# Performance work log

Measured on AMD Instinct MI355X. Metric: run time of the kernel, lower is better.

The kernel has to match this reference:

```python
import jax, jax.numpy as jnp
import numpy as np

N = 50000   # nodes
E = 800000  # edges
F = 256     # input features
H = 256     # hidden units
L = 128     # n_labels
EPS = 1e-5


def setup_inputs():
    key = jax.random.key(0)
    ks = jax.random.split(key, 17)
    s = 0.05
    return {
        "features": jax.random.normal(ks[0], (N, F), jnp.float32),
        "edge_vals": jax.random.uniform(ks[1], (E,), jnp.float32),
        "W1": jax.random.normal(ks[2], (F, H), jnp.float32) * s,
        "db1": jax.random.normal(ks[3], (H,), jnp.float32) * s,
        "b1": jax.random.normal(ks[4], (H,), jnp.float32) * s,
        "g1": jax.random.uniform(ks[5], (H,), jnp.float32, 0.5, 1.5),
        "be1": jax.random.normal(ks[6], (H,), jnp.float32) * s,
        "W2": jax.random.normal(ks[7], (H, H), jnp.float32) * s,
        "b2": jax.random.normal(ks[8], (H,), jnp.float32) * s,
        "g2": jax.random.uniform(ks[9], (H,), jnp.float32, 0.5, 1.5),
        "be2": jax.random.normal(ks[10], (H,), jnp.float32) * s,
        "Wf": jax.random.normal(ks[11], (H, L), jnp.float32) * s,
        "bf": jax.random.normal(ks[12], (L,), jnp.float32) * s,
        "edge_rows": jax.random.randint(ks[13], (E,), 0, N, jnp.int32),
        "edge_cols": jax.random.randint(ks[14], (E,), 0, N, jnp.int32),
        "idx": jax.random.randint(ks[15], (N // 2,), 0, N, jnp.int32),
    }


def _spmm(edge_vals, rows, cols, x):
    # out[i] = sum_{(i,j) in E} A[i,j] * x[j]  (COO sparse @ dense)
    return jax.ops.segment_sum(edge_vals[:, None] * x[cols], rows, num_segments=N)


def _bn(x, gamma, beta):
    # training-mode BatchNormalization: batch (population) stats over nodes
    m = jnp.mean(x, axis=0)
    v = jnp.var(x, axis=0)
    return (x - m) * jax.lax.rsqrt(v + EPS) * gamma + beta


def reference(features, edge_vals, W1, db1, b1, g1, be1, W2, b2, g2, be2, Wf, bf,
              edge_rows, edge_cols, idx):
    # layer 1 (Dense has bias only for l == 0)
    h = features @ W1 + db1
    h = _spmm(edge_vals, edge_rows, edge_cols, h) + b1
    h = jax.nn.relu(_bn(h, g1, be1))
    # layer 2 (no dense bias)
    h = h @ W2
    h = _spmm(edge_vals, edge_rows, edge_cols, h) + b2
    h = jax.nn.relu(_bn(h, g2, be2))
    # dropout = identity (deterministic baseline); final dense head
    out = h @ Wf + bf
    return out[idx]
```

## Files before the change

kernel.cpp:

```cpp
#include <hip/hip_runtime.h>
#include <stdint.h>

#define NN 50000
#define EE 800000
#define FF 256
#define HH 256
#define LL 128
#define SBLK 1024
#define CSRCAP 1000448

typedef __bf16 bf16x8 __attribute__((ext_vector_type(8)));
typedef float  f32x4  __attribute__((ext_vector_type(4)));
typedef unsigned int u32x2 __attribute__((ext_vector_type(2)));
typedef unsigned int u32x4 __attribute__((ext_vector_type(4)));

typedef __attribute__((address_space(1))) unsigned int uint_as1;
typedef __attribute__((address_space(3))) unsigned int uint_as3;

__device__ __forceinline__ unsigned short f2bf(float f) {
  union { float f; unsigned int u; } v; v.f = f;
  unsigned int u = v.u;
  u += 0x7FFFu + ((u >> 16) & 1u);
  return (unsigned short)(u >> 16);
}

__device__ __forceinline__ float bf2f(unsigned short u) {
  union { unsigned int u; float f; } v;
  v.u = ((unsigned int)u) << 16;
  return v.f;
}

__device__ __forceinline__ f32x4 bf4_to_f32(ushort4 u) {
  f32x4 r;
  r.x = bf2f(u.x); r.y = bf2f(u.y); r.z = bf2f(u.z); r.w = bf2f(u.w);
  return r;
}

__device__ __forceinline__ void gload_lds16(const void* g, void* l) {
  __builtin_amdgcn_global_load_lds((const uint_as1*)g, (uint_as3*)l, 16, 0, 0);
}

__global__ __launch_bounds__(256) void k_setup(const int* __restrict__ erows,
                                               int* __restrict__ cnt,
                                               const float* __restrict__ features,
                                               unsigned short* __restrict__ Xb,
                                               const float* __restrict__ W1,
                                               unsigned short* __restrict__ W1t,
                                               const float* __restrict__ W2,
                                               unsigned short* __restrict__ W2t,
                                               const float* __restrict__ Wf,
                                               unsigned short* __restrict__ Wft) {
  __shared__ float tl[64 * 65];
  int b = blockIdx.x, t = threadIdx.x;
  if (b < 3125) {
    int i = b * 256 + t;
    if (i < EE) atomicAdd(&cnt[erows[i]], 1);
  } else if (b < 15625) {
    int i = (b - 3125) * 256 + t;
    f32x4 x = ((const f32x4*)features)[i];
    ushort4 o;
    o.x = f2bf(x.x); o.y = f2bf(x.y); o.z = f2bf(x.z); o.w = f2bf(x.w);
    ((ushort4*)Xb)[i] = o;
  } else {
    int tt = b - 15625;
    const float* in;
    unsigned short* out;
    int Nin, k0, n0;
    if (tt < 16) {
      in = W1; out = W1t; Nin = HH;
      k0 = (tt >> 2) * 64; n0 = (tt & 3) * 64;
    } else if (tt < 32) {
      in = W2; out = W2t; Nin = HH;
      tt -= 16; k0 = (tt >> 2) * 64; n0 = (tt & 3) * 64;
    } else {
      in = Wf; out = Wft; Nin = LL;
      tt -= 32; k0 = (tt >> 1) * 64; n0 = (tt & 1) * 64;
    }
#pragma unroll
    for (int j = 0; j < 16; ++j) {
      int idx = j * 256 + t;
      int r = idx >> 6, c = idx & 63;
      tl[r * 65 + c] = in[(size_t)(k0 + r) * Nin + n0 + c];
    }
    __syncthreads();
#pragma unroll
    for (int j = 0; j < 16; ++j) {
      int idx = j * 256 + t;
      int r = idx >> 6, c = idx & 63;
      out[(size_t)(n0 + r) * HH + k0 + c] = f2bf(tl[c * 65 + r]);
    }
  }
}

__global__ __launch_bounds__(256) void k_alloc(const int* __restrict__ cnt,
                                               int* __restrict__ cursor,
                                               int* __restrict__ total, int n) {
  int i = blockIdx.x * 256 + threadIdx.x;
  int lane = threadIdx.x & 63;
  int c = (i < n) ? ((cnt[i] + 3) & ~3) : 0;
  int incl = c;
#pragma unroll
  for (int off = 1; off < 64; off <<= 1) {
    int v = __shfl_up(incl, off, 64);
    if (lane >= off) incl += v;
  }
  int excl = incl - c;
  int wtot = __shfl(incl, 63, 64);
  int base = 0;
  if (lane == 0) base = atomicAdd(total, wtot);
  base = __shfl(base, 0, 64);
  if (i < n) cursor[i] = base + excl;
}

__global__ __launch_bounds__(256, 3) void k_l1(const unsigned short* __restrict__ A,
                                               const unsigned short* __restrict__ Bt,
                                               const float* __restrict__ bias,
                                               unsigned short* __restrict__ C,
                                               int M, int K, int Nn,
                                               const int* __restrict__ rows,
                                               const int* __restrict__ cols,
                                               const float* __restrict__ vals,
                                               int* __restrict__ cursor,
                                               unsigned int* __restrict__ csr, int E) {
  __shared__ unsigned short lA[128 * 64];
  __shared__ unsigned short lB[128 * 64];
  const int b = blockIdx.x;
  const int tid = threadIdx.x;
  if (b & 1) {
    for (int i = (b >> 1) * 256 + tid; i < E; i += 782 * 256) {
      int p = atomicAdd(&cursor[rows[i]], 1);
      csr[p] = ((unsigned int)cols[i] << 16) | (unsigned int)f2bf(vals[i]);
    }
    return;
  }
  const int gb = b >> 1;
  const int m0 = (gb % 391) * 128, n0 = (gb / 391) * 128;
  const int wave = tid >> 6, lane = tid & 63;
  const int wm = (wave >> 1) * 64, wn = (wave & 1) * 64;
  const int lhi = lane >> 4, llo = lane & 15;
  const int srow = lane >> 3;
  const int scol = (lane & 7) * 8;
  const unsigned short *pA[4], *pB[4];
#pragma unroll
  for (int j = 0; j < 4; ++j) {
    int base = (wave * 4 + j) * 8 + srow;
    int ar = m0 + base;
    ar = ar < M ? ar : 0;
    pA[j] = A + (size_t)ar * K + scol;
    pB[j] = Bt + (size_t)(n0 + base) * K + scol;
  }
  f32x4 zero = {0.f, 0.f, 0.f, 0.f};
  f32x4 acc[4][4];
#pragma unroll
  for (int i = 0; i < 4; ++i)
#pragma unroll
    for (int j = 0; j < 4; ++j) acc[i][j] = zero;
  for (int k0 = 0; k0 < K; k0 += 64) {
#pragma unroll
    for (int j = 0; j < 4; ++j) {
      gload_lds16(pA[j] + k0, lA + (wave * 4 + j) * 8 * 64);
      gload_lds16(pB[j] + k0, lB + (wave * 4 + j) * 8 * 64);
    }
    __syncthreads();
    bf16x8 af[2][4], bfv[2][4];
#pragma unroll
    for (int ks = 0; ks < 2; ++ks) {
#pragma unroll
      for (int mt = 0; mt < 4; ++mt)
        af[ks][mt] = *(const bf16x8*)(lA + (wm + mt * 16 + llo) * 64 + ks * 32 + lhi * 8);
#pragma unroll
      for (int nt = 0; nt < 4; ++nt)
        bfv[ks][nt] = *(const bf16x8*)(lB + (wn + nt * 16 + llo) * 64 + ks * 32 + lhi * 8);
    }
#pragma unroll
    for (int ks = 0; ks < 2; ++ks)
#pragma unroll
      for (int mt = 0; mt < 4; ++mt)
#pragma unroll
        for (int nt = 0; nt < 4; ++nt)
          acc[mt][nt] = __builtin_amdgcn_mfma_f32_16x16x32_bf16(af[ks][mt], bfv[ks][nt], acc[mt][nt], 0, 0, 0);
    __syncthreads();
  }
#pragma unroll
  for (int nt = 0; nt < 4; ++nt) {
    int cn = n0 + wn + nt * 16 + llo;
    float bv = bias[cn];
    unsigned short* Cs = C + (size_t)(cn >> 5) * ((size_t)NN * 32) + (cn & 31);
#pragma unroll
    for (int mt = 0; mt < 4; ++mt) {
      int cm0 = m0 + wm + mt * 16 + lhi * 4;
#pragma unroll
      for (int r = 0; r < 4; ++r) {
        int cm = cm0 + r;
        if (cm < M) Cs[(size_t)cm * 32] = f2bf(acc[mt][nt][r] + bv);
      }
    }
  }
}

__global__ __launch_bounds__(256) void k_spmm(const unsigned short* __restrict__ X,
                                              const int* __restrict__ endp,
                                              const int* __restrict__ cnt,
                                              const unsigned int* __restrict__ csr,
                                              unsigned short* __restrict__ Y, int n) {
  const int slice = blockIdx.x & 7;
  const int rb = blockIdx.x >> 3;
  const int wave = threadIdx.x >> 6, lane = threadIdx.x & 63;
  const int grp = lane >> 3;
  const int cl = lane & 7;
  const unsigned short* Xs = X + (size_t)slice * ((size_t)NN * 32) + cl * 4;
  const int row = rb * 32 + wave * 8 + grp;
  int q = 0, e4 = 0;
  if (row < n) {
    const int c = cnt[row];
    q = endp[row] - c;
    e4 = q + ((c + 3) & ~3);
  }
  f32x4 a0 = {0.f, 0.f, 0.f, 0.f}, a1 = a0, a2 = a0, a3 = a0;
  auto quad = [&](u32x4 cq) {
    const ushort4 x0 = *(const ushort4*)(Xs + ((size_t)(cq.x >> 16) << 5));
    const ushort4 x1 = *(const ushort4*)(Xs + ((size_t)(cq.y >> 16) << 5));
    const ushort4 x2 = *(const ushort4*)(Xs + ((size_t)(cq.z >> 16) << 5));
    const ushort4 x3 = *(const ushort4*)(Xs + ((size_t)(cq.w >> 16) << 5));
    a0 += bf2f((unsigned short)cq.x) * bf4_to_f32(x0);
    a1 += bf2f((unsigned short)cq.y) * bf4_to_f32(x1);
    a2 += bf2f((unsigned short)cq.z) * bf4_to_f32(x2);
    a3 += bf2f((unsigned short)cq.w) * bf4_to_f32(x3);
  };
  if (q < e4) {
    u32x4 cq = __builtin_nontemporal_load((const u32x4*)(csr + q));
    for (q += 4; q < e4; q += 4) {
      u32x4 cn = __builtin_nontemporal_load((const u32x4*)(csr + q));
      quad(cq);
      cq = cn;
    }
    quad(cq);
  }
  if (row < n) {
    const f32x4 a = (a0 + a1) + (a2 + a3);
    u32x2 o;
    o.x = ((unsigned int)f2bf(a.y) << 16) | (unsigned int)f2bf(a.x);
    o.y = ((unsigned int)f2bf(a.w) << 16) | (unsigned int)f2bf(a.z);
    __builtin_nontemporal_store(o, (u32x2*)(Y + (size_t)row * HH + slice * 32 + cl * 4));
  }
}

__global__ __launch_bounds__(256) void k_bnstats(const unsigned short* __restrict__ X,
                                                 float* __restrict__ part, int n) {
  __shared__ float red[4][64][9];
  const int w = threadIdx.x >> 6, l = threadIdx.x & 63;
  f32x4 s = {0.f, 0.f, 0.f, 0.f}, s2 = {0.f, 0.f, 0.f, 0.f};
  for (int r = blockIdx.x * 4 + w; r < n; r += gridDim.x * 4) {
    f32x4 v = bf4_to_f32(((const ushort4*)(X + (size_t)r * HH))[l]);
    s += v;
    s2 += v * v;
  }
#pragma unroll
  for (int j = 0; j < 4; ++j) { red[w][l][j] = s[j]; red[w][l][4 + j] = s2[j]; }
  __syncthreads();
  if (threadIdx.x < 64) {
    int ll = threadIdx.x;
#pragma unroll
    for (int j = 0; j < 8; ++j) {
      float v = red[0][ll][j] + red[1][ll][j] + red[2][ll][j] + red[3][ll][j];
      int c = ll * 4 + (j & 3);
      part[((j < 4) ? 0 : (SBLK * 256)) + blockIdx.x * 256 + c] = v;
    }
  }
}

__global__ __launch_bounds__(256) void k_bnred(const float* __restrict__ part,
                                               float* __restrict__ sums) {
  int c = threadIdx.x;
  int stat = blockIdx.x >> 3, chunk = blockIdx.x & 7;
  const float* p = part + stat * (SBLK * 256) + chunk * 128 * 256;
  float s0 = 0.f, s1 = 0.f, s2 = 0.f, s3 = 0.f;
  for (int b = 0; b < 128; b += 4) {
    s0 += p[(b + 0) * 256 + c];
    s1 += p[(b + 1) * 256 + c];
    s2 += p[(b + 2) * 256 + c];
    s3 += p[(b + 3) * 256 + c];
  }
  atomicAdd(&sums[stat * HH + c], (s0 + s1) + (s2 + s3));
}

__global__ __launch_bounds__(256) void k_bnrc(const unsigned short* __restrict__ X,
                                              const float* __restrict__ sums,
                                              const float* __restrict__ g,
                                              const float* __restrict__ be,
                                              unsigned short* __restrict__ out, int n4) {
  __shared__ float sc[HH], sh[HH];
  int t = threadIdx.x;
  {
    float inv = 1.f / (float)NN;
    float mean = sums[t] * inv;
    float var = sums[HH + t] * inv - mean * mean;
    float s = g[t] * rsqrtf(var + 1e-5f);
    sc[t] = s;
    sh[t] = be[t] - mean * s;
  }
  __syncthreads();
  for (int i = blockIdx.x * 256 + t; i < n4; i += gridDim.x * 256) {
    f32x4 x = bf4_to_f32(((const ushort4*)X)[i]);
    int c0 = (i * 4) & (HH - 1);
    ushort4 o;
    o.x = f2bf(fmaxf(x.x * sc[c0 + 0] + sh[c0 + 0], 0.f));
    o.y = f2bf(fmaxf(x.y * sc[c0 + 1] + sh[c0 + 1], 0.f));
    o.z = f2bf(fmaxf(x.z * sc[c0 + 2] + sh[c0 + 2], 0.f));
    o.w = f2bf(fmaxf(x.w * sc[c0 + 3] + sh[c0 + 3], 0.f));
    ((ushort4*)out)[i] = o;
  }
}

__global__ __launch_bounds__(256) void k_bnrc_pack(const unsigned short* __restrict__ X,
                                                   const float* __restrict__ sums,
                                                   const float* __restrict__ g,
                                                   const float* __restrict__ be,
                                                   const int* __restrict__ idx,
                                                   unsigned short* __restrict__ out) {
  __shared__ float sc[HH], sh[HH];
  int t = threadIdx.x;
  {
    float inv = 1.f / (float)NN;
    float mean = sums[t] * inv;
    float var = sums[HH + t] * inv - mean * mean;
    float s = g[t] * rsqrtf(var + 1e-5f);
    sc[t] = s;
    sh[t] = be[t] - mean * s;
  }
  __syncthreads();
  int i = blockIdx.x * 256 + t;
  int orow = i >> 6;
  int c0 = (i & 63) * 4;
  int irow = idx[orow];
  f32x4 x = bf4_to_f32(*(const ushort4*)(X + (size_t)irow * HH + c0));
  ushort4 o;
  o.x = f2bf(fmaxf(x.x * sc[c0 + 0] + sh[c0 + 0], 0.f));
  o.y = f2bf(fmaxf(x.y * sc[c0 + 1] + sh[c0 + 1], 0.f));
  o.z = f2bf(fmaxf(x.z * sc[c0 + 2] + sh[c0 + 2], 0.f));
  o.w = f2bf(fmaxf(x.w * sc[c0 + 3] + sh[c0 + 3], 0.f));
  ((ushort4*)out)[i] = o;
}

template <int OUTB>
__global__ __launch_bounds__(256, 3) void k_gemm(const unsigned short* __restrict__ A,
                                                 const unsigned short* __restrict__ Bt,
                                                 const float* __restrict__ bias,
                                                 void* __restrict__ Cv,
                                                 int M, int K, int Nn) {
  __shared__ unsigned short lA[128 * 64];
  __shared__ unsigned short lB[128 * 64];
  const int tid = threadIdx.x;
  const int wave = tid >> 6, lane = tid & 63;
  const int m0 = blockIdx.x * 128, n0 = blockIdx.y * 128;
  const int wm = (wave >> 1) * 64, wn = (wave & 1) * 64;
  const int lhi = lane >> 4, llo = lane & 15;
  const int srow = lane >> 3;
  const int scol = (lane & 7) * 8;
  const unsigned short *pA[4], *pB[4];
#pragma unroll
  for (int j = 0; j < 4; ++j) {
    int base = (wave * 4 + j) * 8 + srow;
    int ar = m0 + base;
    ar = ar < M ? ar : 0;
    pA[j] = A + (size_t)ar * K + scol;
    pB[j] = Bt + (size_t)(n0 + base) * K + scol;
  }
  f32x4 zero = {0.f, 0.f, 0.f, 0.f};
  f32x4 acc[4][4];
#pragma unroll
  for (int i = 0; i < 4; ++i)
#pragma unroll
    for (int j = 0; j < 4; ++j) acc[i][j] = zero;
  for (int k0 = 0; k0 < K; k0 += 64) {
#pragma unroll
    for (int j = 0; j < 4; ++j) {
      gload_lds16(pA[j] + k0, lA + (wave * 4 + j) * 8 * 64);
      gload_lds16(pB[j] + k0, lB + (wave * 4 + j) * 8 * 64);
    }
    __syncthreads();
    bf16x8 af[2][4], bfv[2][4];
#pragma unroll
    for (int ks = 0; ks < 2; ++ks) {
#pragma unroll
      for (int mt = 0; mt < 4; ++mt)
        af[ks][mt] = *(const bf16x8*)(lA + (wm + mt * 16 + llo) * 64 + ks * 32 + lhi * 8);
#pragma unroll
      for (int nt = 0; nt < 4; ++nt)
        bfv[ks][nt] = *(const bf16x8*)(lB + (wn + nt * 16 + llo) * 64 + ks * 32 + lhi * 8);
    }
#pragma unroll
    for (int ks = 0; ks < 2; ++ks)
#pragma unroll
      for (int mt = 0; mt < 4; ++mt)
#pragma unroll
        for (int nt = 0; nt < 4; ++nt)
          acc[mt][nt] = __builtin_amdgcn_mfma_f32_16x16x32_bf16(af[ks][mt], bfv[ks][nt], acc[mt][nt], 0, 0, 0);
    __syncthreads();
  }
#pragma unroll
  for (int nt = 0; nt < 4; ++nt) {
    int cn = n0 + wn + nt * 16 + llo;
    float bv = bias ? bias[cn] : 0.f;
#pragma unroll
    for (int mt = 0; mt < 4; ++mt) {
      int cm0 = m0 + wm + mt * 16 + lhi * 4;
#pragma unroll
      for (int r = 0; r < 4; ++r) {
        int cm = cm0 + r;
        if (cm < M) {
          float v = acc[mt][nt][r] + bv;
          if (OUTB)
            ((unsigned short*)Cv)[(size_t)(cn >> 5) * ((size_t)NN * 32) +
                                  (size_t)cm * 32 + (cn & 31)] = f2bf(v);
          else
            ((float*)Cv)[(size_t)cm * Nn + cn] = v;
        }
      }
    }
  }
}

extern "C" void kernel_launch(void* const* d_in, const int* in_sizes, int n_in,
                              void* d_out, int out_size, void* d_ws, size_t ws_size,
                              hipStream_t stream) {
  const float* features = (const float*)d_in[0];
  const float* edge_vals = (const float*)d_in[1];
  const float* W1 = (const float*)d_in[2];
  const float* db1 = (const float*)d_in[3];
  const float* g1 = (const float*)d_in[5];
  const float* be1 = (const float*)d_in[6];
  const float* W2 = (const float*)d_in[7];
  const float* g2 = (const float*)d_in[9];
  const float* be2 = (const float*)d_in[10];
  const float* Wf = (const float*)d_in[11];
  const float* bfb = (const float*)d_in[12];
  const int* erows = (const int*)d_in[13];
  const int* ecols = (const int*)d_in[14];
  const int* idx = (const int*)d_in[15];
  const int M3 = in_sizes[15];
  (void)n_in; (void)out_size; (void)ws_size;

  char* ws = (char*)d_ws;
  size_t off = 0;
  auto alloc = [&](size_t bytes) -> void* {
    void* p = (void*)(ws + off);
    off += (bytes + 255) & ~(size_t)255;
    return p;
  };
  unsigned short* Xb = (unsigned short*)alloc((size_t)NN * HH * 2);
  unsigned short* Ab = (unsigned short*)alloc((size_t)NN * HH * 2);
  unsigned short* Yb = (unsigned short*)alloc((size_t)NN * HH * 2);
  unsigned short* Pb = (unsigned short*)alloc((size_t)25000 * HH * 2);
  unsigned short* W1t = (unsigned short*)alloc((size_t)FF * HH * 2);
  unsigned short* W2t = (unsigned short*)alloc((size_t)HH * HH * 2);
  unsigned short* Wft = (unsigned short*)alloc((size_t)HH * LL * 2);
  int* cursor = (int*)alloc((size_t)NN * 4);
  int* cnt = (int*)alloc((size_t)NN * 4);
  unsigned int* csr = (unsigned int*)alloc((size_t)CSRCAP * 4);
  float* part = (float*)alloc((size_t)2 * SBLK * 256 * 4);
  float* stats = (float*)alloc(4 * HH * 4 + 256);
  float* sums1 = stats;
  float* sums2 = stats + 2 * HH;
  int* total = (int*)(stats + 4 * HH);

  hipMemsetAsync(cnt, 0, (size_t)NN * 4, stream);
  hipMemsetAsync(csr, 0, (size_t)CSRCAP * 4, stream);
  hipMemsetAsync(stats, 0, 4 * HH * 4 + 256, stream);

  k_setup<<<15665, 256, 0, stream>>>(erows, cnt, features, Xb, W1, W1t, W2, W2t, Wf, Wft);
  k_alloc<<<(NN + 255) / 256, 256, 0, stream>>>(cnt, cursor, total, NN);

  k_l1<<<1564, 256, 0, stream>>>(Xb, W1t, db1, Ab, NN, FF, HH,
                                 erows, ecols, edge_vals, cursor, csr, EE);
  k_spmm<<<8 * ((NN + 31) / 32), 256, 0, stream>>>(Ab, cursor, cnt, csr, Yb, NN);
  k_bnstats<<<SBLK, 256, 0, stream>>>(Yb, part, NN);
  k_bnred<<<16, 256, 0, stream>>>(part, sums1);
  k_bnrc<<<2048, 256, 0, stream>>>(Yb, sums1, g1, be1, Xb, NN * HH / 4);

  k_gemm<1><<<dim3((NN + 127) / 128, HH / 128), 256, 0, stream>>>(Xb, W2t, nullptr, Ab, NN, HH, HH);
  k_spmm<<<8 * ((NN + 31) / 32), 256, 0, stream>>>(Ab, cursor, cnt, csr, Yb, NN);
  k_bnstats<<<SBLK, 256, 0, stream>>>(Yb, part, NN);
  k_bnred<<<16, 256, 0, stream>>>(part, sums2);
  k_bnrc_pack<<<(M3 * 64) / 256, 256, 0, stream>>>(Yb, sums2, g2, be2, idx, Pb);

  k_gemm<0><<<dim3((M3 + 127) / 128, LL / 128), 256, 0, stream>>>(Pb, Wft, bfb, d_out, M3, HH, LL);
}
```

Measured before the change: 495.9 us.

## Pad CSR rows to 8 and make SpMM grid-stride with row prefetch

After: 501.3 us. No clear change (+1.1%).

```diff
diff --git a/kernel.cpp b/kernel.cpp
--- a/kernel.cpp
+++ b/kernel.cpp
@@ -7,7 +7,7 @@
 #define HH 256
 #define LL 128
 #define SBLK 1024
-#define CSRCAP 1000448
+#define CSRCAP 1200128
 
 typedef __bf16 bf16x8 __attribute__((ext_vector_type(8)));
 typedef float  f32x4  __attribute__((ext_vector_type(4)));
@@ -97,7 +97,7 @@
                                                int* __restrict__ total, int n) {
   int i = blockIdx.x * 256 + threadIdx.x;
   int lane = threadIdx.x & 63;
-  int c = (i < n) ? ((cnt[i] + 3) & ~3) : 0;
+  int c = (i < n) ? ((cnt[i] + 7) & ~7) : 0;
   int incl = c;
 #pragma unroll
   for (int off = 1; off < 64; off <<= 1) {
@@ -204,44 +204,68 @@
                                               const unsigned int* __restrict__ csr,
                                               unsigned short* __restrict__ Y, int n) {
   const int slice = blockIdx.x & 7;
-  const int rb = blockIdx.x >> 3;
+  const int S = gridDim.x >> 3;
+  const int NRB = (n + 31) >> 5;
   const int wave = threadIdx.x >> 6, lane = threadIdx.x & 63;
   const int grp = lane >> 3;
   const int cl = lane & 7;
   const unsigned short* Xs = X + (size_t)slice * ((size_t)NN * 32) + cl * 4;
-  const int row = rb * 32 + wave * 8 + grp;
-  int q = 0, e4 = 0;
-  if (row < n) {
+
+  int rb = blockIdx.x >> 3;
+  int row = rb * 32 + wave * 8 + grp;
+  int q = 0, e = 0;
+  if (rb < NRB && row < n) {
     const int c = cnt[row];
     q = endp[row] - c;
-    e4 = q + ((c + 3) & ~3);
-  }
-  f32x4 a0 = {0.f, 0.f, 0.f, 0.f}, a1 = a0, a2 = a0, a3 = a0;
-  auto quad = [&](u32x4 cq) {
-    const ushort4 x0 = *(const ushort4*)(Xs + ((size_t)(cq.x >> 16) << 5));
-    const ushort4 x1 = *(const ushort4*)(Xs + ((size_t)(cq.y >> 16) << 5));
-    const ushort4 x2 = *(const ushort4*)(Xs + ((size_t)(cq.z >> 16) << 5));
-    const ushort4 x3 = *(const ushort4*)(Xs + ((size_t)(cq.w >> 16) << 5));
-    a0 += bf2f((unsigned short)cq.x) * bf4_to_f32(x0);
-    a1 += bf2f((unsigned short)cq.y) * bf4_to_f32(x1);
-    a2 += bf2f((unsigned short)cq.z) * bf4_to_f32(x2);
-    a3 += bf2f((unsigned short)cq.w) * bf4_to_f32(x3);
-  };
-  if (q < e4) {
-    u32x4 cq = __builtin_nontemporal_load((const u32x4*)(csr + q));
-    for (q += 4; q < e4; q += 4) {
-      u32x4 cn = __builtin_nontemporal_load((const u32x4*)(csr + q));
-      quad(cq);
-      cq = cn;
-    }
-    quad(cq);
-  }
-  if (row < n) {
-    const f32x4 a = (a0 + a1) + (a2 + a3);
-    u32x2 o;
-    o.x = ((unsigned int)f2bf(a.y) << 16) | (unsigned int)f2bf(a.x);
-    o.y = ((unsigned int)f2bf(a.w) << 16) | (unsigned int)f2bf(a.z);
-    __builtin_nontemporal_store(o, (u32x2*)(Y + (size_t)row * HH + slice * 32 + cl * 4));
+    e = q + ((c + 7) & ~7);
+  }
+  while (rb < NRB) {
+    const int rb2 = rb + S;
+    const int row2 = rb2 * 32 + wave * 8 + grp;
+    int q2 = 0, e2 = 0;
+    if (rb2 < NRB && row2 < n) {
+      const int c = cnt[row2];
+      q2 = endp[row2] - c;
+      e2 = q2 + ((c + 7) & ~7);
+    }
+    f32x4 a0 = {0.f, 0.f, 0.f, 0.f}, a1 = a0, a2 = a0, a3 = a0;
+    auto oct = [&](u32x4 ca, u32x4 cb) {
+      const ushort4 x0 = *(const ushort4*)(Xs + ((size_t)(ca.x >> 16) << 5));
+      const ushort4 x1 = *(const ushort4*)(Xs + ((size_t)(ca.y >> 16) << 5));
+      const ushort4 x2 = *(const ushort4*)(Xs + ((size_t)(ca.z >> 16) << 5));
+      const ushort4 x3 = *(const ushort4*)(Xs + ((size_t)(ca.w >> 16) << 5));
+      const ushort4 x4 = *(const ushort4*)(Xs + ((size_t)(cb.x >> 16) << 5));
+      const ushort4 x5 = *(const ushort4*)(Xs + ((size_t)(cb.y >> 16) << 5));
+      const ushort4 x6 = *(const ushort4*)(Xs + ((size_t)(cb.z >> 16) << 5));
+      const ushort4 x7 = *(const ushort4*)(Xs + ((size_t)(cb.w >> 16) << 5));
+      a0 += bf2f((unsigned short)ca.x) * bf4_to_f32(x0);
+      a1 += bf2f((unsigned short)ca.y) * bf4_to_f32(x1);
+      a2 += bf2f((unsigned short)ca.z) * bf4_to_f32(x2);
+      a3 += bf2f((unsigned short)ca.w) * bf4_to_f32(x3);
+      a0 += bf2f((unsigned short)cb.x) * bf4_to_f32(x4);
+      a1 += bf2f((unsigned short)cb.y) * bf4_to_f32(x5);
+      a2 += bf2f((unsigned short)cb.z) * bf4_to_f32(x6);
+      a3 += bf2f((unsigned short)cb.w) * bf4_to_f32(x7);
+    };
+    if (q < e) {
+      u32x4 ca = __builtin_nontemporal_load((const u32x4*)(csr + q));
+      u32x4 cb = __builtin_nontemporal_load((const u32x4*)(csr + q + 4));
+      for (q += 8; q < e; q += 8) {
+        u32x4 na = __builtin_nontemporal_load((const u32x4*)(csr + q));
+        u32x4 nb = __builtin_nontemporal_load((const u32x4*)(csr + q + 4));
+        oct(ca, cb);
+        ca = na; cb = nb;
+      }
+      oct(ca, cb);
+    }
+    if (row < n) {
+      const f32x4 a = (a0 + a1) + (a2 + a3);
+      u32x2 o;
+      o.x = ((unsigned int)f2bf(a.y) << 16) | (unsigned int)f2bf(a.x);
+      o.y = ((unsigned int)f2bf(a.w) << 16) | (unsigned int)f2bf(a.z);
+      __builtin_nontemporal_store(o, (u32x2*)(Y + (size_t)row * HH + slice * 32 + cl * 4));
+    }
+    rb = rb2; row = row2; q = q2; e = e2;
   }
 }
 
@@ -473,13 +497,13 @@
 
   k_l1<<<1564, 256, 0, stream>>>(Xb, W1t, db1, Ab, NN, FF, HH,
                                  erows, ecols, edge_vals, cursor, csr, EE);
-  k_spmm<<<8 * ((NN + 31) / 32), 256, 0, stream>>>(Ab, cursor, cnt, csr, Yb, NN);
+  k_spmm<<<8 * 391, 256, 0, stream>>>(Ab, cursor, cnt, csr, Yb, NN);
   k_bnstats<<<SBLK, 256, 0, stream>>>(Yb, part, NN);
   k_bnred<<<16, 256, 0, stream>>>(part, sums1);
   k_bnrc<<<2048, 256, 0, stream>>>(Yb, sums1, g1, be1, Xb, NN * HH / 4);
 
   k_gemm<1><<<dim3((NN + 127) / 128, HH / 128), 256, 0, stream>>>(Xb, W2t, nullptr, Ab, NN, HH, HH);
-  k_spmm<<<8 * ((NN + 31) / 32), 256, 0, stream>>>(Ab, cursor, cnt, csr, Yb, NN);
+  k_spmm<<<8 * 391, 256, 0, stream>>>(Ab, cursor, cnt, csr, Yb, NN);
   k_bnstats<<<SBLK, 256, 0, stream>>>(Yb, part, NN);
   k_bnred<<<16, 256, 0, stream>>>(part, sums2);
   k_bnrc_pack<<<(M3 * 64) / 256, 256, 0, stream>>>(Yb, sums2, g2, be2, idx, Pb);
```
